# Performance work log

Hardware: AMD Instinct MI355X
Metric: run time of the kernel (lower is better)

The kernel has to match this reference:

```python
import jax, jax.numpy as jnp
import numpy as np

# ---- architecture constants (match init_kwargs) ----
T, B, NA, OUT = 10, 32, 512, 128          # n_tiles, batch, atoms per sample, output_dim
HID, LMAX = 64, 3                          # hidden_dim, hidden_lmax
IN_MULS = [32, 16, 16, 16]                 # input multiplicity per l (32x0e+16x1o+16x2e+16x3o)
HID_MULS = [HID] * (LMAX + 1)              # gate_irreps multiplicities (64 per l)
DIMS = [2 * l + 1 for l in range(LMAX + 1)]
D_IN = sum(m * d for m, d in zip(IN_MULS, DIMS))   # 272
L0_OUT = HID * (LMAX + 1)                  # 256: scalars(64) + gates(192) in linear_irreps l=0 block


def setup_inputs() -> dict:
    key = jax.random.key(0)
    ks = jax.random.split(key, 12)
    inp = {
        "atom_features": jax.random.normal(ks[0], (B, NA, D_IN), jnp.float32),
        "W0_0": jax.random.normal(ks[1], (T, IN_MULS[0], L0_OUT), jnp.float32),
        "W0_1": jax.random.normal(ks[2], (T, IN_MULS[1], HID), jnp.float32),
        "W0_2": jax.random.normal(ks[3], (T, IN_MULS[2], HID), jnp.float32),
        "W0_3": jax.random.normal(ks[4], (T, IN_MULS[3], HID), jnp.float32),
        "W1_0": jax.random.normal(ks[5], (T, HID, L0_OUT), jnp.float32),
        "W1_1": jax.random.normal(ks[6], (T, HID, HID), jnp.float32),
        "W1_2": jax.random.normal(ks[7], (T, HID, HID), jnp.float32),
        "W1_3": jax.random.normal(ks[8], (T, HID, HID), jnp.float32),
        "Wout": jax.random.normal(ks[9], (T, HID, OUT), jnp.float32),
        "mlp_mapping": jax.random.randint(ks[10], (B, NA, 1), 0, 11),  # 10 == ghost
    }
    return inp


def _split(x, muls):
    """Split flat irreps feature (N, D) into per-l blocks (N, mul_l, 2l+1)."""
    blocks, off = [], 0
    for l, m in enumerate(muls):
        d = 2 * l + 1
        blocks.append(x[:, off:off + m * d].reshape(-1, m, d))
        off += m * d
    return blocks


def _linear(blocks, Ws):
    """e3nn block-diagonal Linear: mix multiplicities per l, 1/sqrt(fan_in) norm."""
    return [jnp.einsum('nmi,mo->noi', b, w) * (1.0 / np.sqrt(b.shape[1]))
            for b, w in zip(blocks, Ws)]


def _gate(blocks):
    """e3nn Gate: SiLU on scalars, SiLU(gates) multiplies each gated l>0 irrep."""
    y0 = blocks[0][..., 0]                      # (N, 256)
    scalars = jax.nn.silu(y0[:, :HID])          # (N, 64)
    gates = jax.nn.silu(y0[:, HID:])            # (N, 192) -> one gate set per l=1..3
    out = [scalars[:, :, None]]
    for l in range(1, LMAX + 1):
        g = gates[:, (l - 1) * HID: l * HID]    # (N, 64)
        out.append(blocks[l] * g[:, :, None])
    return out


def _class_mlp(x, W0s, W1s, Wout_i):
    """Per-class EquivariantMLP (dropout = identity in eval mode)."""
    b = _split(x, IN_MULS)
    b = _gate(_linear(b, W0s))                  # layer 1: Linear -> Gate
    b = _gate(_linear(b, W1s))                  # layer 2: Linear -> Gate
    s = b[0][..., 0]                            # scalar (0e) channels (N, 64)
    return (s @ Wout_i) * (1.0 / np.sqrt(HID))  # readout to OUT scalars


def reference(atom_features, W0_0, W0_1, W0_2, W0_3, W1_0, W1_1, W1_2, W1_3, Wout, mlp_mapping):
    mapping = mlp_mapping[..., 0]               # (B, NA)
    x = atom_features.reshape(B * NA, D_IN)
    outs = []
    for i in range(T):                          # small fixed expert loop
        W0s = [W0_0[i], W0_1[i], W0_2[i], W0_3[i]]
        W1s = [W1_0[i], W1_1[i], W1_2[i], W1_3[i]]
        y = _class_mlp(x, W0s, W1s, Wout[i]).reshape(B, NA, OUT)
        mask = (mapping == i).astype(y.dtype)   # class-i dispatch (ghost id 10 never matches)
        outs.append(jnp.sum(y * mask[..., None], axis=1))  # scatter-sum per batch row
    return jnp.concatenate(outs, axis=1)        # (B, T*OUT)
```

## Files before the change

kernel.cpp:

```cpp
#include <hip/hip_runtime.h>


#define NCLS  10
#define NB    32
#define NATOM 512
#define DIN   272

__global__ __launch_bounds__(256) void eqmlp_fused(
    const float* __restrict__ x,
    const float* __restrict__ W0,
    const float* __restrict__ W1,
    const float* __restrict__ Wo,
    const int*   __restrict__ mapping,
    float*       __restrict__ out)
{
    const int c    = blockIdx.x;
    const int b    = blockIdx.y;
    const int tid  = threadIdx.x;
    const int w    = tid >> 6;
    const int lane = tid & 63;

    __shared__ __align__(16) float W0s[32 * 64];
    __shared__ __align__(16) float W1s[64 * 64];
    __shared__ __align__(16) float xbuf [4][32 * 4];
    __shared__ __align__(16) float h1buf[4][64 * 4];
    __shared__ __align__(16) float hsum[4][64];
    __shared__ __align__(16) float fin[2][128];

    const int* map_b = mapping + b * NATOM;
    const int  mv0 = map_b[w * 128 + lane];
    const int  mv1 = map_b[w * 128 + 64 + lane];

    {
        const float4* g0 = (const float4*)(W0 + (size_t)c * 32 * 256);
        float4* s0 = (float4*)W0s;
        for (int i = tid; i < 32 * 64 / 4; i += 256)
            s0[i] = g0[(i >> 4) * 64 + (i & 15)];
        const float4* g1 = (const float4*)(W1 + (size_t)c * 64 * 256);
        float4* s1 = (float4*)W1s;
        for (int i = tid; i < 64 * 64 / 4; i += 256)
            s1[i] = g1[(i >> 4) * 64 + (i & 15)];
    }
    __syncthreads();

    float zacc = 0.f;

    const float* x_b = x + (size_t)b * NATOM * DIN;
    const float  sc0 = 0.17677669529663689f;
    const float  sc1 = 0.125f;

    for (int chunk = 0; chunk < 2; ++chunk) {
        const int base = w * 128 + chunk * 64;
        unsigned long long mask = __ballot((chunk ? mv1 : mv0) == c);

        while (mask) {
            int a0 = 0, a1 = 0, a2 = 0, a3 = 0, na = 0;
            {             int p = __builtin_ctzll(mask); mask &= mask - 1; a0 = base + p; na = 1; }
            if (mask)   { int p = __builtin_ctzll(mask); mask &= mask - 1; a1 = base + p; na = 2; }
            if (mask)   { int p = __builtin_ctzll(mask); mask &= mask - 1; a2 = base + p; na = 3; }
            if (mask)   { int p = __builtin_ctzll(mask); mask &= mask - 1; a3 = base + p; na = 4; }

            {
                const int m  = lane & 31;
                const int jh = lane >> 5;
                const int e0 = jh ? a1 : a0;
                const int e1 = jh ? a3 : a2;
                float v0 = (jh     < na) ? x_b[(size_t)e0 * DIN + m] : 0.f;
                float v1 = (jh + 2 < na) ? x_b[(size_t)e1 * DIN + m] : 0.f;
                xbuf[w][m * 4 + jh]     = v0;
                xbuf[w][m * 4 + jh + 2] = v1;
            }
            __builtin_amdgcn_wave_barrier();

            float h0 = 0.f, h1 = 0.f, h2 = 0.f, h3 = 0.f;
            #pragma unroll
            for (int m = 0; m < 32; ++m) {
                float  wv = W0s[m * 64 + lane];
                float4 xv = *(const float4*)&xbuf[w][m * 4];
                h0 += xv.x * wv; h1 += xv.y * wv; h2 += xv.z * wv; h3 += xv.w * wv;
            }
            h0 *= sc0; h1 *= sc0; h2 *= sc0; h3 *= sc0;
            h0 = h0 / (1.f + __expf(-h0));
            h1 = h1 / (1.f + __expf(-h1));
            h2 = h2 / (1.f + __expf(-h2));
            h3 = h3 / (1.f + __expf(-h3));
            *(float4*)&h1buf[w][lane * 4] = make_float4(h0, h1, h2, h3);
            __builtin_amdgcn_wave_barrier();

            float z0 = 0.f, z1 = 0.f, z2 = 0.f, z3 = 0.f;
            #pragma unroll
            for (int m = 0; m < 64; ++m) {
                float  wv = W1s[m * 64 + lane];
                float4 hv = *(const float4*)&h1buf[w][m * 4];
                z0 += hv.x * wv; z1 += hv.y * wv; z2 += hv.z * wv; z3 += hv.w * wv;
            }
            z0 *= sc1; z1 *= sc1; z2 *= sc1; z3 *= sc1;
            zacc += z0 / (1.f + __expf(-z0));
            zacc += z1 / (1.f + __expf(-z1));
            zacc += z2 / (1.f + __expf(-z2));
            zacc += z3 / (1.f + __expf(-z3));
            __builtin_amdgcn_wave_barrier();
        }
    }

    hsum[w][lane] = zacc;
    __syncthreads();
    if (tid < 64)
        hsum[0][tid] += hsum[1][tid] + hsum[2][tid] + hsum[3][tid];
    __syncthreads();

    const int col  = tid & 127;
    const int half = tid >> 7;
    const float* Wo_c = Wo + (size_t)c * 64 * 128 + col;
    float acc = 0.f;
    #pragma unroll
    for (int mm = 0; mm < 32; mm += 4) {
        const int m = half * 32 + mm;
        float4 hv = *(const float4*)&hsum[0][m];
        acc += hv.x * Wo_c[(size_t)(m + 0) * 128];
        acc += hv.y * Wo_c[(size_t)(m + 1) * 128];
        acc += hv.z * Wo_c[(size_t)(m + 2) * 128];
        acc += hv.w * Wo_c[(size_t)(m + 3) * 128];
    }
    fin[half][col] = acc;
    __syncthreads();
    if (tid < 128)
        out[(size_t)b * (NCLS * 128) + c * 128 + tid]
            = (fin[0][tid] + fin[1][tid]) * 0.125f;
}

extern "C" void kernel_launch(void* const* d_in, const int* in_sizes, int n_in,
                              void* d_out, int out_size, void* d_ws, size_t ws_size,
                              hipStream_t stream) {
    const float* x  = (const float*)d_in[0];
    const float* W0 = (const float*)d_in[1];
    const float* W1 = (const float*)d_in[5];
    const float* Wo = (const float*)d_in[9];
    const int*   mp = (const int*)  d_in[10];
    float* outp = (float*)d_out;

    dim3 grid(NCLS, NB);
    eqmlp_fused<<<grid, 256, 0, stream>>>(x, W0, W1, Wo, mp, outp);
}
```

Before: 98.87 us.

## Compact matching atoms into shared list and balance groups across waves with prefetch

Builds a compacted shared-memory list of the atoms mapped to this class using ballots and a prefix sum over wave counts. Groups of four atoms are then assigned round-robin to the four waves, which evens out work that was previously fixed to each wave's 128-atom slice and skewed by the random mapping. The next group's x values are prefetched into registers while the current group is being computed, to hide global load latency. This adds two extra block barriers and a small serial prefix sum.

Measured after the change: 93.26 us. 1.06x faster.

```diff
diff --git a/kernel.cpp b/kernel.cpp
--- a/kernel.cpp
+++ b/kernel.cpp
@@ -26,6 +26,8 @@
     __shared__ __align__(16) float h1buf[4][64 * 4];
     __shared__ __align__(16) float hsum[4][64];
     __shared__ __align__(16) float fin[2][128];
+    __shared__ int alist[NATOM];
+    __shared__ int scnt[8], soff[8], stotal;
 
     const int* map_b = mapping + b * NATOM;
     const int  mv0 = map_b[w * 128 + lane];
@@ -41,66 +43,90 @@
         for (int i = tid; i < 64 * 64 / 4; i += 256)
             s1[i] = g1[(i >> 4) * 64 + (i & 15)];
     }
+
+    const unsigned long long bal0 = __ballot(mv0 == c);
+    const unsigned long long bal1 = __ballot(mv1 == c);
+    if (lane == 0) {
+        scnt[w * 2]     = (int)__popcll(bal0);
+        scnt[w * 2 + 1] = (int)__popcll(bal1);
+    }
     __syncthreads();
+    if (tid == 0) {
+        int s = 0;
+        #pragma unroll
+        for (int i = 0; i < 8; ++i) { soff[i] = s; s += scnt[i]; }
+        stotal = s;
+    }
+    __syncthreads();
+    {
+        const unsigned long long lt = (1ull << lane) - 1ull;
+        if (mv0 == c) alist[soff[w * 2]     + (int)__popcll(bal0 & lt)] = w * 128 + lane;
+        if (mv1 == c) alist[soff[w * 2 + 1] + (int)__popcll(bal1 & lt)] = w * 128 + 64 + lane;
+    }
+    __syncthreads();
+    const int total   = stotal;
+    const int ngroups = (total + 3) >> 2;
 
     float zacc = 0.f;
-
     const float* x_b = x + (size_t)b * NATOM * DIN;
     const float  sc0 = 0.17677669529663689f;
     const float  sc1 = 0.125f;
+    const int    m   = lane & 31;
+    const int    jh  = lane >> 5;
 
-    for (int chunk = 0; chunk < 2; ++chunk) {
-        const int base = w * 128 + chunk * 64;
-        unsigned long long mask = __ballot((chunk ? mv1 : mv0) == c);
+    float v0 = 0.f, v1 = 0.f;
+    if (w < ngroups) {
+        int s0 = w * 4 + jh, s1 = s0 + 2;
+        int e0 = (s0 < total) ? alist[s0] : -1;
+        int e1 = (s1 < total) ? alist[s1] : -1;
+        v0 = (e0 >= 0) ? x_b[(size_t)e0 * DIN + m] : 0.f;
+        v1 = (e1 >= 0) ? x_b[(size_t)e1 * DIN + m] : 0.f;
+    }
 
-        while (mask) {
-            int a0 = 0, a1 = 0, a2 = 0, a3 = 0, na = 0;
-            {             int p = __builtin_ctzll(mask); mask &= mask - 1; a0 = base + p; na = 1; }
-            if (mask)   { int p = __builtin_ctzll(mask); mask &= mask - 1; a1 = base + p; na = 2; }
-            if (mask)   { int p = __builtin_ctzll(mask); mask &= mask - 1; a2 = base + p; na = 3; }
-            if (mask)   { int p = __builtin_ctzll(mask); mask &= mask - 1; a3 = base + p; na = 4; }
+    for (int g = w; g < ngroups; g += 4) {
+        xbuf[w][m * 4 + jh]     = v0;
+        xbuf[w][m * 4 + jh + 2] = v1;
 
-            {
-                const int m  = lane & 31;
-                const int jh = lane >> 5;
-                const int e0 = jh ? a1 : a0;
-                const int e1 = jh ? a3 : a2;
-                float v0 = (jh     < na) ? x_b[(size_t)e0 * DIN + m] : 0.f;
-                float v1 = (jh + 2 < na) ? x_b[(size_t)e1 * DIN + m] : 0.f;
-                xbuf[w][m * 4 + jh]     = v0;
-                xbuf[w][m * 4 + jh + 2] = v1;
-            }
-            __builtin_amdgcn_wave_barrier();
+        float nv0 = 0.f, nv1 = 0.f;
+        if (g + 4 < ngroups) {
+            int s0 = (g + 4) * 4 + jh, s1 = s0 + 2;
+            int e0 = (s0 < total) ? alist[s0] : -1;
+            int e1 = (s1 < total) ? alist[s1] : -1;
+            nv0 = (e0 >= 0) ? x_b[(size_t)e0 * DIN + m] : 0.f;
+            nv1 = (e1 >= 0) ? x_b[(size_t)e1 * DIN + m] : 0.f;
+        }
+        __builtin_amdgcn_wave_barrier();
 
-            float h0 = 0.f, h1 = 0.f, h2 = 0.f, h3 = 0.f;
-            #pragma unroll
-            for (int m = 0; m < 32; ++m) {
-                float  wv = W0s[m * 64 + lane];
-                float4 xv = *(const float4*)&xbuf[w][m * 4];
-                h0 += xv.x * wv; h1 += xv.y * wv; h2 += xv.z * wv; h3 += xv.w * wv;
-            }
-            h0 *= sc0; h1 *= sc0; h2 *= sc0; h3 *= sc0;
-            h0 = h0 / (1.f + __expf(-h0));
-            h1 = h1 / (1.f + __expf(-h1));
-            h2 = h2 / (1.f + __expf(-h2));
-            h3 = h3 / (1.f + __expf(-h3));
-            *(float4*)&h1buf[w][lane * 4] = make_float4(h0, h1, h2, h3);
-            __builtin_amdgcn_wave_barrier();
+        float h0 = 0.f, h1 = 0.f, h2 = 0.f, h3 = 0.f;
+        #pragma unroll
+        for (int mm = 0; mm < 32; ++mm) {
+            float  wv = W0s[mm * 64 + lane];
+            float4 xv = *(const float4*)&xbuf[w][mm * 4];
+            h0 += xv.x * wv; h1 += xv.y * wv; h2 += xv.z * wv; h3 += xv.w * wv;
+        }
+        h0 *= sc0; h1 *= sc0; h2 *= sc0; h3 *= sc0;
+        h0 = h0 / (1.f + __expf(-h0));
+        h1 = h1 / (1.f + __expf(-h1));
+        h2 = h2 / (1.f + __expf(-h2));
+        h3 = h3 / (1.f + __expf(-h3));
+        *(float4*)&h1buf[w][lane * 4] = make_float4(h0, h1, h2, h3);
+        __builtin_amdgcn_wave_barrier();
 
-            float z0 = 0.f, z1 = 0.f, z2 = 0.f, z3 = 0.f;
-            #pragma unroll
-            for (int m = 0; m < 64; ++m) {
-                float  wv = W1s[m * 64 + lane];
-                float4 hv = *(const float4*)&h1buf[w][m * 4];
-                z0 += hv.x * wv; z1 += hv.y * wv; z2 += hv.z * wv; z3 += hv.w * wv;
-            }
-            z0 *= sc1; z1 *= sc1; z2 *= sc1; z3 *= sc1;
-            zacc += z0 / (1.f + __expf(-z0));
-            zacc += z1 / (1.f + __expf(-z1));
-            zacc += z2 / (1.f + __expf(-z2));
-            zacc += z3 / (1.f + __expf(-z3));
-            __builtin_amdgcn_wave_barrier();
+        float z0 = 0.f, z1 = 0.f, z2 = 0.f, z3 = 0.f;
+        #pragma unroll
+        for (int mm = 0; mm < 64; ++mm) {
+            float  wv = W1s[mm * 64 + lane];
+            float4 hv = *(const float4*)&h1buf[w][mm * 4];
+            z0 += hv.x * wv; z1 += hv.y * wv; z2 += hv.z * wv; z3 += hv.w * wv;
         }
+        z0 *= sc1; z1 *= sc1; z2 *= sc1; z3 *= sc1;
+        zacc += z0 / (1.f + __expf(-z0));
+        zacc += z1 / (1.f + __expf(-z1));
+        zacc += z2 / (1.f + __expf(-z2));
+        zacc += z3 / (1.f + __expf(-z3));
+        __builtin_amdgcn_wave_barrier();
+
+        v0 = nv0; v1 = nv1;
     }
 
     hsum[w][lane] = zacc;
@@ -115,12 +141,12 @@
     float acc = 0.f;
     #pragma unroll
     for (int mm = 0; mm < 32; mm += 4) {
-        const int m = half * 32 + mm;
-        float4 hv = *(const float4*)&hsum[0][m];
-        acc += hv.x * Wo_c[(size_t)(m + 0) * 128];
-        acc += hv.y * Wo_c[(size_t)(m + 1) * 128];
-        acc += hv.z * Wo_c[(size_t)(m + 2) * 128];
-        acc += hv.w * Wo_c[(size_t)(m + 3) * 128];
+        const int mr = half * 32 + mm;
+        float4 hv = *(const float4*)&hsum[0][mr];
+        acc += hv.x * Wo_c[(size_t)(mr + 0) * 128];
+        acc += hv.y * Wo_c[(size_t)(mr + 1) * 128];
+        acc += hv.z * Wo_c[(size_t)(mr + 2) * 128];
+        acc += hv.w * Wo_c[(size_t)(mr + 3) * 128];
     }
     fin[half][col] = acc;
     __syncthreads();
```
